# Kernel tuning notes

Hardware: AMD Instinct MI355X
Metric: run time of the kernel (lower is better)

The kernel has to match this reference:

```python
import jax, jax.numpy as jnp
import numpy as np
import math

D_MODEL = 1024
N_HEADS = 16
D_HEAD = 64
D_MLP = 4096
N_LAYERS = 12
INIT_STD = 0.02
EPS = 1e-5
BATCH = 2
SEQ = 2048


def setup_inputs() -> dict:
    key = jax.random.key(0)
    ks = jax.random.split(key, 8)
    attn_std = INIT_STD
    proj_std = INIT_STD / math.sqrt(2 * N_LAYERS)
    return {
        "resid_pre": jax.random.normal(ks[0], (BATCH, SEQ, D_MODEL), jnp.float32),
        "ln1_w": jnp.ones((D_MODEL,), jnp.float32),
        "ln1_b": jnp.zeros((D_MODEL,), jnp.float32),
        "W_Q": attn_std * jax.random.normal(ks[1], (N_HEADS, D_MODEL, D_HEAD), jnp.float32),
        "b_Q": jnp.zeros((N_HEADS, D_HEAD), jnp.float32),
        "W_K": attn_std * jax.random.normal(ks[2], (N_HEADS, D_MODEL, D_HEAD), jnp.float32),
        "b_K": jnp.zeros((N_HEADS, D_HEAD), jnp.float32),
        "W_V": attn_std * jax.random.normal(ks[3], (N_HEADS, D_MODEL, D_HEAD), jnp.float32),
        "b_V": jnp.zeros((N_HEADS, D_HEAD), jnp.float32),
        "W_O": proj_std * jax.random.normal(ks[4], (N_HEADS, D_HEAD, D_MODEL), jnp.float32),
        "b_O": jnp.zeros((D_MODEL,), jnp.float32),
        "ln2_w": jnp.ones((D_MODEL,), jnp.float32),
        "ln2_b": jnp.zeros((D_MODEL,), jnp.float32),
        "W_in": INIT_STD * jax.random.normal(ks[5], (D_MODEL, D_MLP), jnp.float32),
        "b_in": jnp.zeros((D_MLP,), jnp.float32),
        "W_out": proj_std * jax.random.normal(ks[6], (D_MLP, D_MODEL), jnp.float32),
        "b_out": jnp.zeros((D_MODEL,), jnp.float32),
    }


def _layernorm(x, w, b):
    mean = x.mean(-1, keepdims=True)
    var = x.var(-1, keepdims=True)  # unbiased=False
    return (x - mean) / jnp.sqrt(var + EPS) * w + b


def _attention(x, W_Q, b_Q, W_K, b_K, W_V, b_V, W_O, b_O):
    # x: [b, s, d]; W_*: [h, d, k]
    q = jnp.einsum('bsd,hdk->bshk', x, W_Q) + b_Q
    k = jnp.einsum('bsd,hdk->bshk', x, W_K) + b_K
    v = jnp.einsum('bsd,hdk->bshk', x, W_V) + b_V
    scores = jnp.einsum('bqhk,bshk->bhqs', q, k) / math.sqrt(D_HEAD)
    seq = x.shape[1]
    causal = jnp.tril(jnp.ones((seq, seq), bool))
    scores = jnp.where(causal, scores, -jnp.inf)
    pattern = jax.nn.softmax(scores, axis=-1)
    z = jnp.einsum('bhqs,bshk->bqhk', pattern, v)
    return jnp.einsum('bqhk,hkd->bqd', z, W_O) + b_O


def reference(resid_pre, ln1_w, ln1_b, W_Q, b_Q, W_K, b_K, W_V, b_V, W_O, b_O,
              ln2_w, ln2_b, W_in, b_in, W_out, b_out):
    attn_out = _attention(_layernorm(resid_pre, ln1_w, ln1_b),
                          W_Q, b_Q, W_K, b_K, W_V, b_V, W_O, b_O)
    resid_mid = resid_pre + attn_out
    h = _layernorm(resid_mid, ln2_w, ln2_b)
    mlp_out = jnp.matmul(jax.nn.relu(jnp.matmul(h, W_in) + b_in), W_out) + b_out
    return resid_mid + mlp_out
```

## Files before the change

### kernel.cpp

```cpp
#include <hip/hip_runtime.h>
#include <stdint.h>


typedef unsigned short u16;
typedef __bf16 bf16x8 __attribute__((ext_vector_type(8)));
typedef __bf16 bf16x4 __attribute__((ext_vector_type(4)));
typedef __bf16 bf16x2 __attribute__((ext_vector_type(2)));
typedef short  s16x4  __attribute__((ext_vector_type(4)));
typedef float  f32x4  __attribute__((ext_vector_type(4)));

#define QSCALE 0.18033688011112042f

__device__ __forceinline__ float bf2f(unsigned int u) {
  union { unsigned int u; float f; } v; v.u = u << 16; return v.f;
}
__device__ __forceinline__ u16 f2bf(float f) {
  union { float f; unsigned int u; } v; v.f = f;
  unsigned int r = v.u + 0x7FFFu + ((v.u >> 16) & 1u);
  return (u16)(r >> 16);
}
__device__ __forceinline__ unsigned pkbf(float lo, float hi) {
#if __has_builtin(__builtin_amdgcn_cvt_pk_bf16_f32)
  bf16x2 t = __builtin_amdgcn_cvt_pk_bf16_f32(lo, hi);
  return __builtin_bit_cast(unsigned, t);
#else
  return (unsigned)f2bf(lo) | ((unsigned)f2bf(hi) << 16);
#endif
}
__device__ __forceinline__ float loadf(const void* p, size_t i, int isf) {
  return isf ? ((const float*)p)[i] : bf2f(((const u16*)p)[i]);
}

__device__ __forceinline__ f32x4 mfma16(s16x4 a, s16x4 b, f32x4 c) {
#if __has_builtin(__builtin_amdgcn_mfma_f32_16x16x16_bf16)
  return __builtin_amdgcn_mfma_f32_16x16x16_bf16(
      __builtin_bit_cast(bf16x4, a), __builtin_bit_cast(bf16x4, b), c, 0, 0, 0);
#else
  return __builtin_amdgcn_mfma_f32_16x16x16bf16_1k(a, b, c, 0, 0, 0);
#endif
}

__global__ __launch_bounds__(256) void detect_dtype(
    const unsigned int* __restrict__ x, int* __restrict__ flag) {
  __shared__ int cnt;
  if (threadIdx.x == 0) cnt = 0;
  __syncthreads();
  int c = 0;
  for (int i = threadIdx.x; i < 512; i += 256) {
    unsigned int e = (x[i] >> 23) & 0xFFu;
    if (e >= 97u && e <= 157u) c++;
  }
  atomicAdd(&cnt, c);
  __syncthreads();
  if (threadIdx.x == 0) *flag = (cnt > 384) ? 1 : 0;
}

__global__ __launch_bounds__(256) void pack_qkv_tiled(
    const int* __restrict__ flagp,
    const void* __restrict__ Wq, const void* __restrict__ Wk, const void* __restrict__ Wv,
    u16* __restrict__ WT) {
  __shared__ float t[64][65];
  const int isf = *flagp;
  const int tid = threadIdx.x;
  const int mh = blockIdx.y;
  const int mat = mh >> 4, h = mh & 15;
  const int d0 = blockIdx.x << 6;
  const void* src = (mat == 0) ? Wq : (mat == 1) ? Wk : Wv;
  const float scale = (mat == 0) ? QSCALE : 1.f;
  const int lane = tid & 63, rr = tid >> 6;
  const size_t sbase = ((size_t)h << 16) + lane;
#pragma unroll
  for (int i = 0; i < 16; i++) {
    int d = i * 4 + rr;
    t[d][lane] = loadf(src, sbase + (size_t)(d0 + d) * 64, isf) * scale;
  }
  __syncthreads();
#pragma unroll
  for (int i = 0; i < 16; i++) {
    int k = i * 4 + rr;
    WT[((size_t)((mat << 10) + (h << 6) + k) << 10) + d0 + lane] = f2bf(t[lane][k]);
  }
}

__global__ __launch_bounds__(256) void transpose_tiled(
    const int* __restrict__ flagp, const void* __restrict__ src,
    u16* __restrict__ dst, int R, int C) {
  __shared__ float t[64][65];
  const int isf = *flagp;
  const int tid = threadIdx.x;
  const int c0 = blockIdx.x << 6, r0 = blockIdx.y << 6;
  const int lane = tid & 63, rr = tid >> 6;
#pragma unroll
  for (int i = 0; i < 16; i++) {
    int r = i * 4 + rr;
    t[r][lane] = loadf(src, (size_t)(r0 + r) * C + c0 + lane, isf);
  }
  __syncthreads();
#pragma unroll
  for (int i = 0; i < 16; i++) {
    int c = i * 4 + rr;
    dst[(size_t)(c0 + c) * R + r0 + lane] = f2bf(t[lane][c]);
  }
}

__global__ __launch_bounds__(256) void pack_biases(
    const int* __restrict__ flagp,
    const void* bq, const void* bk, const void* bv,
    const void* bO, const void* bin, const void* bout,
    float* __restrict__ out) {
  const int isf = *flagp;
  int i = blockIdx.x * 256 + threadIdx.x;
  float v;
  if (i < 1024)      v = loadf(bq,   i,        isf) * QSCALE;
  else if (i < 2048) v = loadf(bk,   i - 1024, isf);
  else if (i < 3072) v = loadf(bv,   i - 2048, isf);
  else if (i < 4096) v = loadf(bO,   i - 3072, isf);
  else if (i < 8192) v = loadf(bin,  i - 4096, isf);
  else               v = loadf(bout, i - 8192, isf);
  out[i] = v;
}

template<int SRC>
__global__ __launch_bounds__(256) void ln_fwd(
    const int* __restrict__ flagp, const void* __restrict__ xin,
    const void* __restrict__ w, const void* __restrict__ b,
    u16* __restrict__ out) {
  const int isf = *flagp;
  const int row = blockIdx.x, tid = threadIdx.x;
  const int col = tid << 2;
  const size_t base = ((size_t)row << 10) + col;
  float v[4];
#pragma unroll
  for (int i = 0; i < 4; i++)
    v[i] = (SRC == 1) ? ((const float*)xin)[base + i] : loadf(xin, base + i, isf);
  float s  = v[0] + v[1] + v[2] + v[3];
  float ss = v[0]*v[0] + v[1]*v[1] + v[2]*v[2] + v[3]*v[3];
#pragma unroll
  for (int mk = 32; mk >= 1; mk >>= 1) {
    s  += __shfl_xor(s,  mk, 64);
    ss += __shfl_xor(ss, mk, 64);
  }
  __shared__ float red[8];
  if ((tid & 63) == 0) { red[tid >> 6] = s; red[4 + (tid >> 6)] = ss; }
  __syncthreads();
  float S  = red[0] + red[1] + red[2] + red[3];
  float SS = red[4] + red[5] + red[6] + red[7];
  float mean = S * (1.f / 1024.f);
  float var  = SS * (1.f / 1024.f) - mean * mean;
  float rstd = rsqrtf(var + 1e-5f);
  u16 e[4];
#pragma unroll
  for (int i = 0; i < 4; i++) {
    float wv = loadf(w, col + i, isf);
    float bv = loadf(b, col + i, isf);
    e[i] = f2bf((v[i] - mean) * rstd * wv + bv);
  }
  uint2 o;
  o.x = (unsigned)e[0] | ((unsigned)e[1] << 16);
  o.y = (unsigned)e[2] | ((unsigned)e[3] << 16);
  *(uint2*)(out + base) = o;
}

template<int MODE, int TM, int KW>
__global__ __launch_bounds__(KW * 256) void gemm_bt(
    const int* __restrict__ flagp,
    const u16* __restrict__ A, const u16* __restrict__ BT,
    const float* __restrict__ bias, const void* __restrict__ resid,
    void* __restrict__ out, void* __restrict__ out2, void* __restrict__ out3,
    int M, int N, int K, int SHL) {
  constexpr int WR = TM / 32;
  constexpr int ASZ = TM * 32;
  constexpr int BSZ = 128 * 32;
  constexpr int STAGE_B = KW * (ASZ + BSZ) * 2;
  constexpr int RED_B = (KW > 1) ? TM * 132 * 4 : 1;
  constexpr int SMEM_B = STAGE_B > RED_B ? STAGE_B : RED_B;
  __shared__ __align__(16) char smem[SMEM_B];
  u16* as = (u16*)smem;
  u16* bs = (u16*)smem + KW * ASZ;

  int isf = 0;
  if (MODE == 2 || MODE == 3) isf = *flagp;
  const int Lb = blockIdx.x;
  const int xcd = Lb & 7, sidx = Lb >> 3;
  const int SH = 1 << SHL;
  const int by = xcd * SH + (sidx & (SH - 1));
  const int bx = sidx >> SHL;
  const int tid = threadIdx.x;
  const int L = tid & 63, w = tid >> 6;
  const int g = w >> 2, wl = w & 3;
  const int wm = (wl >> 1) * (TM >> 1), wn = (wl & 1) << 6;
  const int row0 = by * TM, col0 = bx << 7;
  const int m = L & 15, quad = L >> 4;

  f32x4 zero4 = {0.f, 0.f, 0.f, 0.f};
  f32x4 acc[WR][4];
#pragma unroll
  for (int i = 0; i < WR; i++)
#pragma unroll
    for (int j = 0; j < 4; j++) acc[i][j] = zero4;

  const int KSEG = K / KW;
  const int tl = tid & 255;
  const int tm = tl >> 2;
  const int tk = (tl & 3) << 3;
  const u16* Ag  = A  + (size_t)(row0 + tm) * K + g * KSEG + tk;
  const u16* Ag2 = Ag + (size_t)64 * K;
  const u16* Bg  = BT + (size_t)(col0 + tm) * K + g * KSEG + tk;
  const u16* Bg2 = Bg + (size_t)64 * K;
  u16* asg  = as + g * ASZ;
  u16* bsg  = bs + g * BSZ;
  u16* asl  = asg + tl * 8;
  u16* asl2 = asg + 2048 + tl * 8;
  u16* bsl  = bsg + tl * 8;
  u16* bsl2 = bsg + 2048 + tl * 8;

  const int aoff = (wm + m) * 32 + quad * 8;
  const int boff = (wn + m) * 32 + quad * 8;

  int4 ar0, ar1, br0, br1;
  ar0 = *(const int4*)Ag;
  if (TM == 128) ar1 = *(const int4*)Ag2;
  br0 = *(const int4*)Bg;
  br1 = *(const int4*)Bg2;

  for (int kk = 0; kk < KSEG; kk += 32) {
    __syncthreads();
    *(int4*)asl = ar0;
    if (TM == 128) *(int4*)asl2 = ar1;
    *(int4*)bsl = br0;
    *(int4*)bsl2 = br1;
    __syncthreads();
    if (kk + 32 < KSEG) {
      ar0 = *(const int4*)(Ag + kk + 32);
      if (TM == 128) ar1 = *(const int4*)(Ag2 + kk + 32);
      br0 = *(const int4*)(Bg + kk + 32);
      br1 = *(const int4*)(Bg2 + kk + 32);
    }
    bf16x8 af[WR], bfr[4];
#pragma unroll
    for (int i = 0; i < WR; i++) af[i]  = *(const bf16x8*)&asg[aoff + i * 512];
#pragma unroll
    for (int j = 0; j < 4; j++) bfr[j] = *(const bf16x8*)&bsg[boff + j * 512];
#pragma unroll
    for (int i = 0; i < WR; i++)
#pragma unroll
      for (int j = 0; j < 4; j++)
        acc[i][j] = __builtin_amdgcn_mfma_f32_16x16x32_bf16(af[i], bfr[j], acc[i][j], 0, 0, 0);
  }

  if (KW > 1) {
    __syncthreads();
    float* red = (float*)smem;
    if (g == 1) {
#pragma unroll
      for (int i = 0; i < WR; i++)
#pragma unroll
        for (int j = 0; j < 4; j++)
#pragma unroll
          for (int r = 0; r < 4; r++)
            red[(wm + i * 16 + quad * 4 + r) * 132 + wn + j * 16 + m] = acc[i][j][r];
    }
    __syncthreads();
    if (g == 0) {
#pragma unroll
      for (int i = 0; i < WR; i++)
#pragma unroll
        for (int j = 0; j < 4; j++)
#pragma unroll
          for (int r = 0; r < 4; r++)
            acc[i][j][r] += red[(wm + i * 16 + quad * 4 + r) * 132 + wn + j * 16 + m];
    }
  }

  if (g == 0) {
#pragma unroll
    for (int j = 0; j < 4; j++) {
      const int col = col0 + wn + j * 16 + m;
      const float bval = bias[col];
      if (MODE == 4) {
        const int sel = col >> 10;
        const int hh  = (col >> 6) & 15;
        const int f   = col & 63;
#pragma unroll
        for (int i = 0; i < WR; i++) {
          const int rowb = row0 + wm + i * 16 + quad * 4;
          if (sel < 2) {
            u16* dst = (u16*)(sel ? out2 : out);
#pragma unroll
            for (int r = 0; r < 4; r++)
              dst[((((size_t)hh << 12) + rowb + r) << 6) + f] = f2bf(acc[i][j][r] + bval);
          } else {
            uint2 o;
            o.x = pkbf(acc[i][j][0] + bval, acc[i][j][1] + bval);
            o.y = pkbf(acc[i][j][2] + bval, acc[i][j][3] + bval);
            *(uint2*)&((u16*)out3)[(((size_t)hh * 64 + f) << 12) + rowb] = o;
          }
        }
      } else {
#pragma unroll
        for (int i = 0; i < WR; i++) {
          const int rowb = row0 + wm + i * 16 + quad * 4;
#pragma unroll
          for (int r = 0; r < 4; r++) {
            float vv = acc[i][j][r] + bval;
            size_t idx = (size_t)(rowb + r) * N + col;
            if (MODE == 1) {
              ((u16*)out)[idx] = f2bf(fmaxf(vv, 0.f));
            } else if (MODE == 2) {
              ((float*)out)[idx] = vv + loadf(resid, idx, isf);
            } else if (MODE == 3) {
              float o = vv + ((const float*)resid)[idx];
              if (isf) ((float*)out)[idx] = o;
              else     ((u16*)out)[idx]   = f2bf(o);
            }
          }
        }
      }
    }
  }
}

__global__ __launch_bounds__(512, 4) void attn_part(
    const u16* __restrict__ qh, const u16* __restrict__ kh,
    const u16* __restrict__ vT, u16* __restrict__ Opart,
    float* __restrict__ stats, u16* __restrict__ z) {
  const int combo = blockIdx.x;
  const int qt = blockIdx.y;
  const int ci = blockIdx.z;
  const int q0 = qt << 7;
  const int nc = (q0 + 128 + 1023) >> 10;
  if (ci >= nc) return;
  const int k_lo = ci << 10;
  const int k_hi = min(k_lo + 1024, q0 + 128);
  const int nsteps = (k_hi - k_lo + 127) >> 7;

  __shared__ u16 kS[128 * 72];
  __shared__ u16 vS[64 * 136];
  const int tid = threadIdx.x, L = tid & 63, w = tid >> 6;
  const int m = L & 15, quad = L >> 4;
  const int h = combo >> 1, b = combo & 1;
  const size_t tb = (size_t)b * 2048;
  const size_t hbase = (size_t)h * 4096;
  const int qg = q0 + w * 16 + m;

  bf16x8 qb0, qb1;
  {
    const u16* qp = qh + ((hbase + tb + (size_t)qg) << 6) + quad * 8;
    qb0 = *(const bf16x8*)qp;
    qb1 = *(const bf16x8*)(qp + 32);
  }

  f32x4 zero4 = {0.f, 0.f, 0.f, 0.f};
  f32x4 O[4];
#pragma unroll
  for (int ft = 0; ft < 4; ft++) O[ft] = zero4;
  float mrow = -30000.f, lrow = 0.f;

  const int krow[2] = { (0*512+tid) >> 3, (1*512+tid) >> 3 };
  const int kc = tid & 7;
  const int vf[2] = { (0*512+tid) >> 4, (1*512+tid) >> 4 };
  const int vc = tid & 15;
  const int vq = (vc & 1) << 1;
  const int vk4 = (vc >> 1) << 2;
  const int vc0 = (vq << 5) + vk4;
  const int vc1 = ((vq + 1) << 5) + vk4;

  for (int j = 0; j < nsteps; j++) {
    const int k0 = k_lo + (j << 7);
    int4 kr[2], vr[2];
#pragma unroll
    for (int i = 0; i < 2; i++) {
      kr[i] = *(const int4*)(kh + ((hbase + tb + k0 + krow[i]) << 6) + kc * 8);
      vr[i] = *(const int4*)(vT + (((size_t)h * 64 + vf[i]) << 12) + tb + k0 + vc * 8);
    }
    __syncthreads();
#pragma unroll
    for (int i = 0; i < 2; i++) {
      *(int4*)&kS[krow[i] * 72 + kc * 8] = kr[i];
      union { int4 v; s16x4 hh[2]; } tv; tv.v = vr[i];
      *(s16x4*)&vS[vf[i] * 136 + vc0] = tv.hh[0];
      *(s16x4*)&vS[vf[i] * 136 + vc1] = tv.hh[1];
    }
    __syncthreads();

#pragma unroll
    for (int hs = 0; hs < 2; hs++) {
      const int kbase = k0 + hs * 64;
      f32x4 sc[4];
#pragma unroll
      for (int kt4 = 0; kt4 < 4; kt4++) {
        const int kt = hs * 4 + kt4;
        const u16* kp = &kS[(kt * 16 + m) * 72 + quad * 8];
        bf16x8 ka0 = *(const bf16x8*)kp;
        bf16x8 ka1 = *(const bf16x8*)(kp + 32);
        f32x4 t = zero4;
        t = __builtin_amdgcn_mfma_f32_16x16x32_bf16(ka0, qb0, t, 0, 0, 0);
        t = __builtin_amdgcn_mfma_f32_16x16x32_bf16(ka1, qb1, t, 0, 0, 0);
        sc[kt4] = t;
      }
      if (kbase + 64 > q0) {
#pragma unroll
        for (int kt4 = 0; kt4 < 4; kt4++)
#pragma unroll
          for (int r = 0; r < 4; r++) {
            int ktok = kbase + kt4 * 16 + quad * 4 + r;
            if (ktok > qg) sc[kt4][r] = -30000.f;
          }
      }
      float mx = sc[0][0];
#pragma unroll
      for (int kt4 = 0; kt4 < 4; kt4++)
#pragma unroll
        for (int r = 0; r < 4; r++) mx = fmaxf(mx, sc[kt4][r]);
      mx = fmaxf(mx, __shfl_xor(mx, 16, 64));
      mx = fmaxf(mx, __shfl_xor(mx, 32, 64));
      if (!__all(mx <= mrow + 8.f)) {
        float mnew = fmaxf(mrow, mx);
        float alpha = __builtin_amdgcn_exp2f(mrow - mnew);
        lrow *= alpha;
#pragma unroll
        for (int ft = 0; ft < 4; ft++) O[ft] *= alpha;
        mrow = mnew;
      }
      s16x4 pb[4];
      float sum = 0.f;
#pragma unroll
      for (int kt4 = 0; kt4 < 4; kt4++) {
        float e0 = __builtin_amdgcn_exp2f(sc[kt4][0] - mrow);
        float e1 = __builtin_amdgcn_exp2f(sc[kt4][1] - mrow);
        float e2 = __builtin_amdgcn_exp2f(sc[kt4][2] - mrow);
        float e3 = __builtin_amdgcn_exp2f(sc[kt4][3] - mrow);
        sum += (e0 + e1) + (e2 + e3);
        union { uint2 u; s16x4 hh; } pu;
        pu.u.x = pkbf(e0, e1);
        pu.u.y = pkbf(e2, e3);
        pb[kt4] = pu.hh;
      }
      sum += __shfl_xor(sum, 16, 64);
      sum += __shfl_xor(sum, 32, 64);
      lrow += sum;
#pragma unroll
      for (int ft = 0; ft < 4; ft++) {
        const u16* vp = &vS[(ft * 16 + m) * 136 + quad * 32 + hs * 16];
#pragma unroll
        for (int p2 = 0; p2 < 2; p2++) {
          union { bf16x8 v; s16x4 hh[2]; } u;
          u.v = *(const bf16x8*)(vp + p2 * 8);
          O[ft] = mfma16(u.hh[0], pb[2 * p2],     O[ft]);
          O[ft] = mfma16(u.hh[1], pb[2 * p2 + 1], O[ft]);
        }
      }
    }
  }

  if (nc == 1) {
    float inv = 1.f / lrow;
#pragma unroll
    for (int ft = 0; ft < 4; ft++) O[ft] *= inv;
  }

  __syncthreads();
#pragma unroll
  for (int ft = 0; ft < 4; ft++) {
    union { uint2 u; s16x4 hh; } o4;
    o4.u.x = pkbf(O[ft][0], O[ft][1]);
    o4.u.y = pkbf(O[ft][2], O[ft][3]);
    *(s16x4*)&kS[(w * 16 + m) * 72 + ft * 16 + quad * 4] = o4.hh;
  }
  __syncthreads();
  if (nc == 1) {
    u16* zp = z + ((tb + (size_t)q0) << 10) + h * 64;
#pragma unroll
    for (int it = 0; it < 2; it++) {
      int idx = it * 512 + tid;
      int row = idx >> 3, c = idx & 7;
      *(int4*)&zp[((size_t)row << 10) + c * 8] = *(const int4*)&kS[row * 72 + c * 8];
    }
  } else {
    const int slot = (combo * 16 + qt) * 2 + ci;
    u16* op = Opart + ((size_t)slot << 13);
#pragma unroll
    for (int it = 0; it < 2; it++) {
      int idx = it * 512 + tid;
      int row = idx >> 3, c = idx & 7;
      *(int4*)&op[row * 64 + c * 8] = *(const int4*)&kS[row * 72 + c * 8];
    }
    if (quad == 0) {
      stats[slot * 256 + w * 16 + m]       = mrow;
      stats[slot * 256 + 128 + w * 16 + m] = lrow;
    }
  }
}

__global__ __launch_bounds__(512) void attn_merge(
    const u16* __restrict__ Opart, const float* __restrict__ stats,
    u16* __restrict__ z) {
  const int combo = blockIdx.x, qt = 8 + blockIdx.y;
  const int h = combo >> 1, b = combo & 1;
  const int q0 = qt << 7;
  const int tid = threadIdx.x;
  const int t = tid >> 2, f0 = (tid & 3) << 4;
  const int slot0 = (combo * 16 + qt) * 2;
  float M = fmaxf(stats[slot0 * 256 + t], stats[(slot0 + 1) * 256 + t]);
  float acc[16];
#pragma unroll
  for (int e = 0; e < 16; e++) acc[e] = 0.f;
  float ltot = 0.f;
#pragma unroll
  for (int ci = 0; ci < 2; ci++) {
    float mi = stats[(slot0 + ci) * 256 + t];
    float li = stats[(slot0 + ci) * 256 + 128 + t];
    float wgt = exp2f(mi - M);
    ltot += wgt * li;
    const u16* op = Opart + (((size_t)(slot0 + ci)) << 13) + t * 64 + f0;
    union { int4 v; u16 u[8]; } a0, a1;
    a0.v = *(const int4*)op;
    a1.v = *(const int4*)(op + 8);
#pragma unroll
    for (int e = 0; e < 8; e++) {
      acc[e]     += wgt * bf2f(a0.u[e]);
      acc[8 + e] += wgt * bf2f(a1.u[e]);
    }
  }
  float inv = 1.f / ltot;
  union { int4 v; u16 u[8]; } o0, o1;
#pragma unroll
  for (int e = 0; e < 8; e++) {
    o0.u[e] = f2bf(acc[e] * inv);
    o1.u[e] = f2bf(acc[8 + e] * inv);
  }
  size_t tok = (size_t)b * 2048 + q0 + t;
  *(int4*)&z[tok * 1024 + h * 64 + f0]     = o0.v;
  *(int4*)&z[tok * 1024 + h * 64 + f0 + 8] = o1.v;
}

extern "C" void kernel_launch(void* const* d_in, const int* in_sizes, int n_in,
                              void* d_out, int out_size, void* d_ws, size_t ws_size,
                              hipStream_t stream) {
  (void)in_sizes; (void)n_in; (void)out_size; (void)ws_size;
  const void* resid_pre = d_in[0];
  const void* ln1_w = d_in[1];
  const void* ln1_b = d_in[2];
  const void* W_Q   = d_in[3];
  const void* b_Q   = d_in[4];
  const void* W_K   = d_in[5];
  const void* b_K   = d_in[6];
  const void* W_V   = d_in[7];
  const void* b_V   = d_in[8];
  const void* W_O   = d_in[9];
  const void* b_O   = d_in[10];
  const void* ln2_w = d_in[11];
  const void* ln2_b = d_in[12];
  const void* W_in  = d_in[13];
  const void* b_in  = d_in[14];
  const void* W_out = d_in[15];
  const void* b_out = d_in[16];

  char* p = (char*)d_ws;
  auto alloc = [&](size_t bytes) {
    char* r = p; p += (bytes + 255) & ~(size_t)255; return (void*)r;
  };
  int*   flag      = (int*)  alloc(256);
  u16*   WqkvT     = (u16*)  alloc(3072ull * 1024 * 2);
  u16*   WoT       = (u16*)  alloc(1024ull * 1024 * 2);
  u16*   WinT      = (u16*)  alloc(4096ull * 1024 * 2);
  u16*   WoutT     = (u16*)  alloc(1024ull * 4096 * 2);
  float* biases    = (float*)alloc(9216 * 4);
  u16*   xn        = (u16*)  alloc(4096ull * 1024 * 2);
  u16*   q_hm      = (u16*)  alloc(16ull * 4096 * 64 * 2);
  u16*   k_hm      = (u16*)  alloc(16ull * 4096 * 64 * 2);
  u16*   vTws      = (u16*)  alloc(16ull * 64 * 4096 * 2);
  float* resid_mid = (float*)alloc(4096ull * 1024 * 4);
  u16*   h2        = (u16*)  alloc(4096ull * 1024 * 2);
  u16*   act       = (u16*)  alloc(4096ull * 4096 * 2);
  u16*   z = xn;
  u16*   Opart = act;
  float* stats = (float*)h2;

  detect_dtype<<<1, 256, 0, stream>>>((const unsigned int*)resid_pre, flag);

  pack_qkv_tiled<<<dim3(16, 48), 256, 0, stream>>>(flag, W_Q, W_K, W_V, WqkvT);
  transpose_tiled<<<dim3(16, 16), 256, 0, stream>>>(flag, W_O,   WoT,   1024, 1024);
  transpose_tiled<<<dim3(64, 16), 256, 0, stream>>>(flag, W_in,  WinT,  1024, 4096);
  transpose_tiled<<<dim3(16, 64), 256, 0, stream>>>(flag, W_out, WoutT, 4096, 1024);
  pack_biases<<<36, 256, 0, stream>>>(flag, b_Q, b_K, b_V, b_O, b_in, b_out, biases);

  ln_fwd<0><<<4096, 256, 0, stream>>>(flag, resid_pre, ln1_w, ln1_b, xn);
  gemm_bt<4, 128, 1><<<768, 256, 0, stream>>>(
      flag, xn, WqkvT, biases, nullptr, q_hm, k_hm, vTws, 4096, 3072, 1024, 2);
  attn_part<<<dim3(32, 16, 2), 512, 0, stream>>>(q_hm, k_hm, vTws, Opart, stats, z);
  attn_merge<<<dim3(32, 8), 512, 0, stream>>>(Opart, stats, z);
  gemm_bt<2, 64, 2><<<512, 512, 0, stream>>>(
      flag, z, WoT, biases + 3072, resid_pre, resid_mid, nullptr, nullptr, 4096, 1024, 1024, 3);
  ln_fwd<1><<<4096, 256, 0, stream>>>(flag, resid_mid, ln2_w, ln2_b, h2);
  gemm_bt<1, 128, 1><<<1024, 256, 0, stream>>>(
      flag, h2, WinT, biases + 4096, nullptr, act, nullptr, nullptr, 4096, 4096, 1024, 2);
  gemm_bt<3, 64, 2><<<512, 512, 0, stream>>>(
      flag, act, WoutT, biases + 8192, resid_mid, d_out, nullptr, nullptr, 4096, 1024, 4096, 3);
}
```

Baseline: 414.0 us.

## Double-buffer GEMM tiles with direct global-to-LDS async loads

The GEMM main loop now uses `global_load_lds` to copy A and BT tiles straight from global memory into shared memory, instead of staging them through registers. Two shared-memory buffers per K-group let the next K-step load while the MFMAs run on the current one, and each step needs one barrier instead of two. The cost is twice the LDS footprint per block, which may lower occupancy. Correctness also depends on the barrier draining the outstanding LDS-direct loads before the tile is read.

New measurement: 410.0 us. Within noise of the previous version (-1.0%).

```diff
diff --git a/kernel.cpp b/kernel.cpp
--- a/kernel.cpp
+++ b/kernel.cpp
@@ -29,6 +29,12 @@
 }
 __device__ __forceinline__ float loadf(const void* p, size_t i, int isf) {
   return isf ? ((const float*)p)[i] : bf2f(((const u16*)p)[i]);
+}
+
+__device__ __forceinline__ void load_lds16(const u16* g, u16* l) {
+  __builtin_amdgcn_global_load_lds(
+      (const __attribute__((address_space(1))) void*)g,
+      (__attribute__((address_space(3))) void*)l, 16, 0, 0);
 }
 
 __device__ __forceinline__ f32x4 mfma16(s16x4 a, s16x4 b, f32x4 c) {
@@ -171,12 +177,12 @@
   constexpr int WR = TM / 32;
   constexpr int ASZ = TM * 32;
   constexpr int BSZ = 128 * 32;
-  constexpr int STAGE_B = KW * (ASZ + BSZ) * 2;
+  constexpr int STAGE_B = KW * 2 * (ASZ + BSZ) * 2;
   constexpr int RED_B = (KW > 1) ? TM * 132 * 4 : 1;
   constexpr int SMEM_B = STAGE_B > RED_B ? STAGE_B : RED_B;
   __shared__ __align__(16) char smem[SMEM_B];
   u16* as = (u16*)smem;
-  u16* bs = (u16*)smem + KW * ASZ;
+  u16* bs = as + KW * 2 * ASZ;
 
   int isf = 0;
   if (MODE == 2 || MODE == 3) isf = *flagp;
@@ -200,56 +206,55 @@
     for (int j = 0; j < 4; j++) acc[i][j] = zero4;
 
   const int KSEG = K / KW;
-  const int tl = tid & 255;
-  const int tm = tl >> 2;
-  const int tk = (tl & 3) << 3;
-  const u16* Ag  = A  + (size_t)(row0 + tm) * K + g * KSEG + tk;
-  const u16* Ag2 = Ag + (size_t)64 * K;
-  const u16* Bg  = BT + (size_t)(col0 + tm) * K + g * KSEG + tk;
-  const u16* Bg2 = Bg + (size_t)64 * K;
-  u16* asg  = as + g * ASZ;
-  u16* bsg  = bs + g * BSZ;
-  u16* asl  = asg + tl * 8;
-  u16* asl2 = asg + 2048 + tl * 8;
-  u16* bsl  = bsg + tl * 8;
-  u16* bsl2 = bsg + 2048 + tl * 8;
-
   const int aoff = (wm + m) * 32 + quad * 8;
   const int boff = (wn + m) * 32 + quad * 8;
-
-  int4 ar0, ar1, br0, br1;
-  ar0 = *(const int4*)Ag;
-  if (TM == 128) ar1 = *(const int4*)Ag2;
-  br0 = *(const int4*)Bg;
-  br1 = *(const int4*)Bg2;
-
-  for (int kk = 0; kk < KSEG; kk += 32) {
-    __syncthreads();
-    *(int4*)asl = ar0;
-    if (TM == 128) *(int4*)asl2 = ar1;
-    *(int4*)bsl = br0;
-    *(int4*)bsl2 = br1;
-    __syncthreads();
-    if (kk + 32 < KSEG) {
-      ar0 = *(const int4*)(Ag + kk + 32);
-      if (TM == 128) ar1 = *(const int4*)(Ag2 + kk + 32);
-      br0 = *(const int4*)(Bg + kk + 32);
-      br1 = *(const int4*)(Bg2 + kk + 32);
-    }
+  const int rA = L >> 2, c8 = (L & 3) << 3;
+  constexpr int NA = TM / 64;
+
+  auto stage = [&](int buf, int kk) {
+    u16* asgb = as + ((g << 1) + buf) * ASZ;
+    u16* bsgb = bs + ((g << 1) + buf) * BSZ;
+#pragma unroll
+    for (int c = 0; c < NA; c++) {
+      const u16* gp = A + (size_t)(row0 + wl * 16 * NA + c * 16 + rA) * K
+                        + g * KSEG + kk + c8;
+      load_lds16(gp, asgb + (wl * NA + c) * 512);
+    }
+#pragma unroll
+    for (int c = 0; c < 2; c++) {
+      const u16* gp = BT + (size_t)(col0 + wl * 32 + c * 16 + rA) * K
+                         + g * KSEG + kk + c8;
+      load_lds16(gp, bsgb + (wl * 2 + c) * 512);
+    }
+  };
+
+  auto compute_step = [&](int buf) {
+    const u16* asgb = as + ((g << 1) + buf) * ASZ;
+    const u16* bsgb = bs + ((g << 1) + buf) * BSZ;
     bf16x8 af[WR], bfr[4];
 #pragma unroll
-    for (int i = 0; i < WR; i++) af[i]  = *(const bf16x8*)&asg[aoff + i * 512];
-#pragma unroll
-    for (int j = 0; j < 4; j++) bfr[j] = *(const bf16x8*)&bsg[boff + j * 512];
+    for (int i = 0; i < WR; i++) af[i]  = *(const bf16x8*)&asgb[aoff + i * 512];
+#pragma unroll
+    for (int j = 0; j < 4; j++) bfr[j] = *(const bf16x8*)&bsgb[boff + j * 512];
 #pragma unroll
     for (int i = 0; i < WR; i++)
 #pragma unroll
       for (int j = 0; j < 4; j++)
         acc[i][j] = __builtin_amdgcn_mfma_f32_16x16x32_bf16(af[i], bfr[j], acc[i][j], 0, 0, 0);
+  };
+
+  const int nt = KSEG / 32;
+  stage(0, 0);
+  __syncthreads();
+  int buf = 0;
+  for (int t = 0; t < nt; ++t) {
+    if (t + 1 < nt) stage(buf ^ 1, (t + 1) * 32);
+    compute_step(buf);
+    __syncthreads();
+    buf ^= 1;
   }
 
   if (KW > 1) {
-    __syncthreads();
     float* red = (float*)smem;
     if (g == 1) {
 #pragma unroll
```
